# Optimization experiments

Measured on AMD Instinct MI355X. Metric: run time of the kernel, lower is better.

## Reference

```python
import jax, jax.numpy as jnp
import numpy as np

N = 4096   # patients
D = 256    # encoding dim per modality
EPS = 1e-8 # torch CosineSimilarity eps


def setup_inputs() -> dict:
    key = jax.random.key(0)
    ks = jax.random.split(key, 7)
    return {
        "log_hazard": jax.random.normal(ks[0], (N,), dtype=jnp.float32),
        "time": jax.random.randint(ks[1], (N,), 0, 3650, dtype=jnp.int32),
        "event": jax.random.randint(ks[2], (N,), 0, 2, dtype=jnp.int32),
        "eb0": jax.random.normal(ks[3], (N, D), dtype=jnp.float32),
        "eb1": jax.random.normal(ks[4], (N, D), dtype=jnp.float32),
        "eb2": jax.random.normal(ks[5], (N, D), dtype=jnp.float32),
        "eb3": jax.random.normal(ks[6], (N, D), dtype=jnp.float32),
        "M_margin": 1,
    }


def _cox_npll(h, t, e):
    # risk_matrix = (outer(t,t) >= t^2).T  ->  risk[i,j] = (t_j * t_i >= t_i^2)
    tt = t[:, None] * t[None, :]                      # [N,N] = t_i * t_j
    risk = (tt >= (t * t)[:, None]).astype(h.dtype)   # row i: patients j with t_j >= t_i
    log_denom = jnp.log(risk @ jnp.exp(h))            # [N]
    ef = e.astype(h.dtype)
    return -jnp.sum(ef * (h - log_denom)) / jnp.sum(ef)


def _similarity_loss(blocks, margin):
    # Vectorized form of the O(N^2 * n_mod) pairwise loop.
    matched = jnp.zeros((N, N), dtype=blocks[0].dtype)  # sum_mod cos(x_i, x_j) over valid mods
    own = jnp.zeros((N, N), dtype=blocks[0].dtype)      # sum_mod cos(x_i, x_i) over valid mods
    for x in blocks:
        nrm = jnp.linalg.norm(x, axis=1)                # [N]
        den = jnp.maximum(nrm, EPS)
        xn = x / den[:, None]
        S = xn @ xn.T                                   # cos(x_i, x_j) with torch eps semantics
        diag = (nrm * nrm) / (den * den)                # cos(x_i, x_i)
        miss = jnp.all(x == x[:, :1], axis=1)           # modality missing (constant row)
        valid = (~(miss[:, None] | miss[None, :])).astype(x.dtype)
        matched = matched + valid * S
        own = own + valid * diag[:, None]
    offdiag = 1.0 - jnp.eye(N, dtype=matched.dtype)
    per_pair = jax.nn.relu(margin - matched + own)
    return jnp.sum(offdiag * per_pair)


def reference(log_hazard, time, event, eb0, eb1, eb2, eb3, M_margin):
    margin = jnp.float32(M_margin)
    cox = _cox_npll(log_hazard, time, event)
    sim = _similarity_loss([eb0, eb1, eb2, eb3], margin)
    return cox + sim
```

## Files before the change

### kernel.cpp

```cpp
#include <hip/hip_runtime.h>
#include <stdint.h>

#define NPAT 4096
#define DIM  256
#define EPSV 1e-8f
#define BT   128
#define NT   (NPAT / BT)
#define NBLK (NT * (NT + 1) / 2)
#define NSTEP 16
#define NBINS 4096

typedef float f32x4  __attribute__((ext_vector_type(4)));
typedef float f32x16 __attribute__((ext_vector_type(16)));
typedef int   i32x8  __attribute__((ext_vector_type(8)));

#define WS_DVAL_OFF 256
#define WS_MVEC_OFF (WS_DVAL_OFF + 16*NPAT)
#define WS_XN_OFF   (WS_MVEC_OFF + 16*NPAT)

__device__ __forceinline__ float decode_margin(const int* pm) {
  int v = *pm;
  if (v > -16777216 && v < 16777216) return (float)v;
  return __int_as_float(v);
}

__global__ __launch_bounds__(256) void prep_kernel(
    const float4* __restrict__ eb0, const float4* __restrict__ eb1,
    const float4* __restrict__ eb2, const float4* __restrict__ eb3,
    uint8_t* __restrict__ XnF, float* __restrict__ dval_f,
    float* __restrict__ mvec_f, float* __restrict__ scal)
{
  const int i    = blockIdx.x;
  const int wv   = threadIdx.x >> 6;
  const int lane = threadIdx.x & 63;
  const float4* ebs[4] = {eb0, eb1, eb2, eb3};
  const float4 v = ebs[wv][i * (DIM / 4) + lane];
  float s = v.x * v.x + v.y * v.y + v.z * v.z + v.w * v.w;
#pragma unroll
  for (int o = 32; o; o >>= 1) s += __shfl_down(s, o, 64);
  s = __shfl(s, 0, 64);
  const float x0 = __shfl(v.x, 0, 64);
  const bool eq = (v.x == x0) && (v.y == x0) && (v.z == x0) && (v.w == x0);
  const bool miss = (__ballot(eq) == ~0ull);
  const float nrm = sqrtf(s);
  const float den = fmaxf(nrm, EPSV);
  const float inv = miss ? 0.0f : (1.0f / den);
  int p = 0;
  p = __builtin_amdgcn_cvt_pk_fp8_f32(v.x * inv, v.y * inv, p, false);
  p = __builtin_amdgcn_cvt_pk_fp8_f32(v.z * inv, v.w * inv, p, true);
  const int g  = i >> 5, r = i & 31;
  const int ss = wv * 4 + (lane >> 4);
  const int h  = (lane >> 3) & 1;
  const int b  = (lane & 7) * 4;
  *(int*)&XnF[(size_t)((g * 16 + ss) * 64 + (h * 32 + r)) * 32 + b] = p;
  if (lane == 0) {
    const float diag = (nrm * nrm) / (den * den);
    dval_f[i * 4 + wv] = miss ? 0.0f : diag;
    mvec_f[i * 4 + wv] = miss ? 0.0f : 1.0f;
  }
  if (i == 0 && threadIdx.x == 0) {
    scal[0] = 0.0f;
    scal[1] = 0.0f;
    ((unsigned*)scal)[2] = 0u;
  }
}

__global__ __launch_bounds__(256, 3) void sim_gemm_kernel(
    const uint8_t* __restrict__ XnF, const float4* __restrict__ dval,
    const float4* __restrict__ mvec, const int* __restrict__ pmargin,
    const float* __restrict__ h, const int* __restrict__ t,
    const int* __restrict__ e, float* __restrict__ scal,
    float* __restrict__ out)
{
  __shared__ __align__(16) uint8_t smem[16384 + 256];
  const int L   = blockIdx.x;
  const int tid = threadIdx.x;
  const int lane = tid & 63, wvv = tid >> 6;

  if (L == 0) {
    float* bins = (float*)smem;
    float* wt   = (float*)(smem + 16384);
    float* rn   = (float*)(smem + 16384 + 32);
    float* rd   = (float*)(smem + 16384 + 64);
#pragma unroll
    for (int k = 0; k < 16; ++k) bins[tid + k * 256] = 0.0f;
    __syncthreads();
#pragma unroll
    for (int k = 0; k < 16; ++k) {
      const int i = tid + k * 256;
      atomicAdd(&bins[t[i]], expf(h[i]));
    }
    __syncthreads();
    float seg[16]; float part = 0.0f;
#pragma unroll
    for (int k = 0; k < 16; ++k) { seg[k] = bins[tid * 16 + k]; part += seg[k]; }
    float sfx = part;
#pragma unroll
    for (int off = 1; off < 64; off <<= 1) {
      const float u = __shfl_down(sfx, off, 64);
      if (lane + off < 64) sfx += u;
    }
    if (lane == 0) wt[wvv] = sfx;
    __syncthreads();
    float above = 0.0f;
    for (int w = wvv + 1; w < 4; ++w) above += wt[w];
    float run = above + (sfx - part);
#pragma unroll
    for (int k = 15; k >= 0; --k) { run += seg[k]; bins[tid * 16 + k] = run; }
    __syncthreads();
    float nloc = 0.0f, dloc = 0.0f;
#pragma unroll
    for (int k = 0; k < 16; ++k) {
      const int i = tid + k * 256;
      const float ei = (float)e[i];
      if (ei != 0.0f) { nloc += ei * (h[i] - logf(bins[t[i]])); dloc += ei; }
    }
#pragma unroll
    for (int o = 32; o; o >>= 1) {
      nloc += __shfl_down(nloc, o, 64);
      dloc += __shfl_down(dloc, o, 64);
    }
    if (lane == 0) { rn[wvv] = nloc; rd[wvv] = dloc; }
    __syncthreads();
    if (tid == 0) {
      float n = 0.0f, d = 0.0f;
#pragma unroll
      for (int k = 0; k < 4; ++k) { n += rn[k]; d += rd[k]; }
      atomicExch(&scal[1], n / d);
      __threadfence();
      const unsigned old = atomicAdd(&((unsigned*)scal)[2], 1u);
      if (old == NBLK) {
        __threadfence();
        out[0] = atomicAdd(&scal[0], 0.0f) - (n / d);
      }
    }
    return;
  }

  const int T = L - 1;
  int bi = (int)((2 * NT + 1 - sqrtf((float)((2 * NT + 1) * (2 * NT + 1)) - 8.0f * T)) * 0.5f);
  if (bi < 0) bi = 0;
  if (bi > NT - 1) bi = NT - 1;
  while (bi > 0 && bi * NT - bi * (bi - 1) / 2 > T) --bi;
  while ((bi + 1) * NT - (bi + 1) * bi / 2 <= T) ++bi;
  const int bj = bi + (T - (bi * NT - bi * (bi - 1) / 2));

  const int wi = wvv >> 1, wj = wvv & 1;
  const int gA0 = bi * 4 + wi * 2;
  const int gB0 = bj * 4 + wj * 2;
  const uint8_t* pA = XnF + (size_t)(gA0 * 16) * 2048 + lane * 32;
  const uint8_t* pB = XnF + (size_t)(gB0 * 16) * 2048 + lane * 32;

  f32x16 acc[2][2] = {};

#pragma unroll 2
  for (int s = 0; s < NSTEP; ++s) {
    const i32x8 a0 = *(const i32x8*)(pA + (size_t)s * 2048);
    const i32x8 a1 = *(const i32x8*)(pA + 32768 + (size_t)s * 2048);
    const i32x8 b0 = *(const i32x8*)(pB + (size_t)s * 2048);
    const i32x8 b1 = *(const i32x8*)(pB + 32768 + (size_t)s * 2048);
    acc[0][0] = __builtin_amdgcn_mfma_scale_f32_32x32x64_f8f6f4(
        a0, b0, acc[0][0], 0, 0, 0, 0x7F7F7F7F, 0, 0x7F7F7F7F);
    acc[0][1] = __builtin_amdgcn_mfma_scale_f32_32x32x64_f8f6f4(
        a0, b1, acc[0][1], 0, 0, 0, 0x7F7F7F7F, 0, 0x7F7F7F7F);
    acc[1][0] = __builtin_amdgcn_mfma_scale_f32_32x32x64_f8f6f4(
        a1, b0, acc[1][0], 0, 0, 0, 0x7F7F7F7F, 0, 0x7F7F7F7F);
    acc[1][1] = __builtin_amdgcn_mfma_scale_f32_32x32x64_f8f6f4(
        a1, b1, acc[1][1], 0, 0, 0, 0x7F7F7F7F, 0, 0x7F7F7F7F);
  }

  float4* eRDi = (float4*)smem;
  float4* eCMi = (float4*)smem + BT;
  float4* eRDj = (float4*)smem + 2 * BT;
  float4* eCMj = (float4*)smem + 3 * BT;
  float*  wred = (float*)(smem + 8192);
  if (tid < BT) {
    eRDi[tid] = dval[bi * BT + tid];
    eCMi[tid] = mvec[bi * BT + tid];
  } else {
    const int ss = tid - BT;
    eRDj[ss] = dval[bj * BT + ss];
    eCMj[ss] = mvec[bj * BT + ss];
  }
  __syncthreads();

  const float margin = decode_margin(pmargin);
  const bool isDiag = (bi == bj);
  float local = 0.0f;
  const int colA = lane & 31, hsel = lane >> 5;
#pragma unroll
  for (int mi = 0; mi < 2; ++mi) {
#pragma unroll
    for (int mj = 0; mj < 2; ++mj) {
      const int jl = wj * 64 + mj * 32 + colA;
      const float4 cmj = eCMj[jl];
      const float4 rdj = eRDj[jl];
#pragma unroll
      for (int rr = 0; rr < 16; ++rr) {
        const int il = wi * 64 + mi * 32 + (rr & 3) + 8 * (rr >> 2) + 4 * hsel;
        const float4 rdi = eRDi[il];
        const float sv = acc[mi][mj][rr];
        const float own_ij = rdi.x * cmj.x + rdi.y * cmj.y + rdi.z * cmj.z + rdi.w * cmj.w;
        const float v1 = fmaxf(margin - sv + own_ij, 0.0f);
        local += (isDiag && il == jl) ? 0.0f : v1;
        if (!isDiag) {
          const float4 cmi = eCMi[il];
          const float own_ji = rdj.x * cmi.x + rdj.y * cmi.y + rdj.z * cmi.z + rdj.w * cmi.w;
          local += fmaxf(margin - sv + own_ji, 0.0f);
        }
      }
    }
  }
#pragma unroll
  for (int o = 32; o; o >>= 1) local += __shfl_down(local, o, 64);
  if (lane == 0) wred[wvv] = local;
  __syncthreads();
  if (tid == 0) {
    atomicAdd(&scal[0], wred[0] + wred[1] + wred[2] + wred[3]);
    __threadfence();
    const unsigned old = atomicAdd(&((unsigned*)scal)[2], 1u);
    if (old == NBLK) {
      __threadfence();
      out[0] = atomicAdd(&scal[0], 0.0f) - atomicAdd(&scal[1], 0.0f);
    }
  }
}

extern "C" void kernel_launch(void* const* d_in, const int* in_sizes, int n_in,
                              void* d_out, int out_size, void* d_ws, size_t ws_size,
                              hipStream_t stream) {
  const float* h    = (const float*)d_in[0];
  const int*   t    = (const int*)  d_in[1];
  const int*   e    = (const int*)  d_in[2];
  const float4* eb0 = (const float4*)d_in[3];
  const float4* eb1 = (const float4*)d_in[4];
  const float4* eb2 = (const float4*)d_in[5];
  const float4* eb3 = (const float4*)d_in[6];
  const int*   pm   = (const int*)  d_in[7];

  char*    ws   = (char*)d_ws;
  float*   scal = (float*)ws;
  float*   dvf  = (float*)(ws + WS_DVAL_OFF);
  float*   mvf  = (float*)(ws + WS_MVEC_OFF);
  uint8_t* XnF  = (uint8_t*)(ws + WS_XN_OFF);

  prep_kernel<<<NPAT, 256, 0, stream>>>(eb0, eb1, eb2, eb3, XnF, dvf, mvf, scal);
  sim_gemm_kernel<<<NBLK + 1, 256, 0, stream>>>(XnF, (const float4*)dvf, (const float4*)mvf,
                                                pm, h, t, e, scal, (float*)d_out);
}
```

Before: 109.0 us.

## Use 128x64 rectangular tiles over upper triangle with register double-buffered loads

Measured after the change: 124.1 us. 1.14x slower.

```diff
diff --git a/kernel.cpp b/kernel.cpp
--- a/kernel.cpp
+++ b/kernel.cpp
@@ -4,9 +4,9 @@
 #define NPAT 4096
 #define DIM  256
 #define EPSV 1e-8f
-#define BT   128
-#define NT   (NPAT / BT)
-#define NBLK (NT * (NT + 1) / 2)
+#define NRT  32
+#define NCT  64
+#define NBT  1056
 #define NSTEP 16
 #define NBINS 4096
 
@@ -129,7 +129,7 @@
       atomicExch(&scal[1], n / d);
       __threadfence();
       const unsigned old = atomicAdd(&((unsigned*)scal)[2], 1u);
-      if (old == NBLK) {
+      if (old == NBT) {
         __threadfence();
         out[0] = atomicAdd(&scal[0], 0.0f) - (n / d);
       }
@@ -138,76 +138,74 @@
   }
 
   const int T = L - 1;
-  int bi = (int)((2 * NT + 1 - sqrtf((float)((2 * NT + 1) * (2 * NT + 1)) - 8.0f * T)) * 0.5f);
-  if (bi < 0) bi = 0;
-  if (bi > NT - 1) bi = NT - 1;
-  while (bi > 0 && bi * NT - bi * (bi - 1) / 2 > T) --bi;
-  while ((bi + 1) * NT - (bi + 1) * bi / 2 <= T) ++bi;
-  const int bj = bi + (T - (bi * NT - bi * (bi - 1) / 2));
+  int ri = (int)((65.0f - sqrtf(4225.0f - 4.0f * T)) * 0.5f);
+  if (ri < 0) ri = 0;
+  if (ri > NRT - 1) ri = NRT - 1;
+  while (ri > 0 && ri * (65 - ri) > T) --ri;
+  while ((ri + 1) * (65 - (ri + 1)) <= T) ++ri;
+  const int cj = 2 * ri + (T - ri * (65 - ri));
 
   const int wi = wvv >> 1, wj = wvv & 1;
-  const int gA0 = bi * 4 + wi * 2;
-  const int gB0 = bj * 4 + wj * 2;
+  const int gA0 = ri * 4 + wi * 2;
+  const int gB  = cj * 2 + wj;
   const uint8_t* pA = XnF + (size_t)(gA0 * 16) * 2048 + lane * 32;
-  const uint8_t* pB = XnF + (size_t)(gB0 * 16) * 2048 + lane * 32;
-
-  f32x16 acc[2][2] = {};
-
+  const uint8_t* pB = XnF + (size_t)(gB  * 16) * 2048 + lane * 32;
+
+  f32x16 acc[2] = {};
+  i32x8 af[2][2], bf[2];
+
+  af[0][0] = *(const i32x8*)(pA);
+  af[0][1] = *(const i32x8*)(pA + 32768);
+  bf[0]    = *(const i32x8*)(pB);
 #pragma unroll 2
   for (int s = 0; s < NSTEP; ++s) {
-    const i32x8 a0 = *(const i32x8*)(pA + (size_t)s * 2048);
-    const i32x8 a1 = *(const i32x8*)(pA + 32768 + (size_t)s * 2048);
-    const i32x8 b0 = *(const i32x8*)(pB + (size_t)s * 2048);
-    const i32x8 b1 = *(const i32x8*)(pB + 32768 + (size_t)s * 2048);
-    acc[0][0] = __builtin_amdgcn_mfma_scale_f32_32x32x64_f8f6f4(
-        a0, b0, acc[0][0], 0, 0, 0, 0x7F7F7F7F, 0, 0x7F7F7F7F);
-    acc[0][1] = __builtin_amdgcn_mfma_scale_f32_32x32x64_f8f6f4(
-        a0, b1, acc[0][1], 0, 0, 0, 0x7F7F7F7F, 0, 0x7F7F7F7F);
-    acc[1][0] = __builtin_amdgcn_mfma_scale_f32_32x32x64_f8f6f4(
-        a1, b0, acc[1][0], 0, 0, 0, 0x7F7F7F7F, 0, 0x7F7F7F7F);
-    acc[1][1] = __builtin_amdgcn_mfma_scale_f32_32x32x64_f8f6f4(
-        a1, b1, acc[1][1], 0, 0, 0, 0x7F7F7F7F, 0, 0x7F7F7F7F);
+    const int c = s & 1;
+    if (s < NSTEP - 1) {
+      af[c ^ 1][0] = *(const i32x8*)(pA + (size_t)(s + 1) * 2048);
+      af[c ^ 1][1] = *(const i32x8*)(pA + 32768 + (size_t)(s + 1) * 2048);
+      bf[c ^ 1]    = *(const i32x8*)(pB + (size_t)(s + 1) * 2048);
+    }
+    acc[0] = __builtin_amdgcn_mfma_scale_f32_32x32x64_f8f6f4(
+        af[c][0], bf[c], acc[0], 0, 0, 0, 0x7F7F7F7F, 0, 0x7F7F7F7F);
+    acc[1] = __builtin_amdgcn_mfma_scale_f32_32x32x64_f8f6f4(
+        af[c][1], bf[c], acc[1], 0, 0, 0, 0x7F7F7F7F, 0, 0x7F7F7F7F);
   }
 
   float4* eRDi = (float4*)smem;
-  float4* eCMi = (float4*)smem + BT;
-  float4* eRDj = (float4*)smem + 2 * BT;
-  float4* eCMj = (float4*)smem + 3 * BT;
-  float*  wred = (float*)(smem + 8192);
-  if (tid < BT) {
-    eRDi[tid] = dval[bi * BT + tid];
-    eCMi[tid] = mvec[bi * BT + tid];
-  } else {
-    const int ss = tid - BT;
-    eRDj[ss] = dval[bj * BT + ss];
-    eCMj[ss] = mvec[bj * BT + ss];
+  float4* eCMi = (float4*)smem + 128;
+  float4* eRDj = (float4*)smem + 256;
+  float4* eCMj = (float4*)smem + 320;
+  float*  wred = (float*)(smem + 384 * 16);
+  if (tid < 128) {
+    eRDi[tid] = dval[ri * 128 + tid];
+    eCMi[tid] = mvec[ri * 128 + tid];
+  } else if (tid < 192) {
+    const int ss = tid - 128;
+    eRDj[ss] = dval[cj * 64 + ss];
+    eCMj[ss] = mvec[cj * 64 + ss];
   }
   __syncthreads();
 
   const float margin = decode_margin(pmargin);
-  const bool isDiag = (bi == bj);
   float local = 0.0f;
   const int colA = lane & 31, hsel = lane >> 5;
+  const int jl = wj * 32 + colA;
+  const int jg = cj * 64 + jl;
+  const float4 cmj = eCMj[jl];
+  const float4 rdj = eRDj[jl];
 #pragma unroll
   for (int mi = 0; mi < 2; ++mi) {
 #pragma unroll
-    for (int mj = 0; mj < 2; ++mj) {
-      const int jl = wj * 64 + mj * 32 + colA;
-      const float4 cmj = eCMj[jl];
-      const float4 rdj = eRDj[jl];
-#pragma unroll
-      for (int rr = 0; rr < 16; ++rr) {
-        const int il = wi * 64 + mi * 32 + (rr & 3) + 8 * (rr >> 2) + 4 * hsel;
+    for (int rr = 0; rr < 16; ++rr) {
+      const int il = wi * 64 + mi * 32 + (rr & 3) + 8 * (rr >> 2) + 4 * hsel;
+      const int ig = ri * 128 + il;
+      if (jg > ig) {
         const float4 rdi = eRDi[il];
-        const float sv = acc[mi][mj][rr];
+        const float4 cmi = eCMi[il];
+        const float sv = acc[mi][rr];
         const float own_ij = rdi.x * cmj.x + rdi.y * cmj.y + rdi.z * cmj.z + rdi.w * cmj.w;
-        const float v1 = fmaxf(margin - sv + own_ij, 0.0f);
-        local += (isDiag && il == jl) ? 0.0f : v1;
-        if (!isDiag) {
-          const float4 cmi = eCMi[il];
-          const float own_ji = rdj.x * cmi.x + rdj.y * cmi.y + rdj.z * cmi.z + rdj.w * cmi.w;
-          local += fmaxf(margin - sv + own_ji, 0.0f);
-        }
+        const float own_ji = rdj.x * cmi.x + rdj.y * cmi.y + rdj.z * cmi.z + rdj.w * cmi.w;
+        local += fmaxf(margin - sv + own_ij, 0.0f) + fmaxf(margin - sv + own_ji, 0.0f);
       }
     }
   }
@@ -219,7 +217,7 @@
     atomicAdd(&scal[0], wred[0] + wred[1] + wred[2] + wred[3]);
     __threadfence();
     const unsigned old = atomicAdd(&((unsigned*)scal)[2], 1u);
-    if (old == NBLK) {
+    if (old == NBT) {
       __threadfence();
       out[0] = atomicAdd(&scal[0], 0.0f) - atomicAdd(&scal[1], 0.0f);
     }
@@ -245,6 +243,6 @@
   uint8_t* XnF  = (uint8_t*)(ws + WS_XN_OFF);
 
   prep_kernel<<<NPAT, 256, 0, stream>>>(eb0, eb1, eb2, eb3, XnF, dvf, mvf, scal);
-  sim_gemm_kernel<<<NBLK + 1, 256, 0, stream>>>(XnF, (const float4*)dvf, (const float4*)mvf,
-                                                pm, h, t, e, scal, (float*)d_out);
-}
+  sim_gemm_kernel<<<NBT + 1, 256, 0, stream>>>(XnF, (const float4*)dvf, (const float4*)mvf,
+                                               pm, h, t, e, scal, (float*)d_out);
+}
```

## Use 256x128 rectangular triangular tiles with 512-thread blocks and batched fragment loads

Applied to the files above, without the earlier changes.

Result: slower. 116.5 us (+6.9%).

```diff
diff --git a/kernel.cpp b/kernel.cpp
--- a/kernel.cpp
+++ b/kernel.cpp
@@ -4,9 +4,9 @@
 #define NPAT 4096
 #define DIM  256
 #define EPSV 1e-8f
-#define BT   128
-#define NT   (NPAT / BT)
-#define NBLK (NT * (NT + 1) / 2)
+#define NRT  16
+#define NCT  32
+#define NBT  272
 #define NSTEP 16
 #define NBINS 4096
 
@@ -65,7 +65,7 @@
   }
 }
 
-__global__ __launch_bounds__(256, 3) void sim_gemm_kernel(
+__global__ __launch_bounds__(512, 2) void sim_gemm_kernel(
     const uint8_t* __restrict__ XnF, const float4* __restrict__ dval,
     const float4* __restrict__ mvec, const int* __restrict__ pmargin,
     const float* __restrict__ h, const int* __restrict__ t,
@@ -80,20 +80,20 @@
   if (L == 0) {
     float* bins = (float*)smem;
     float* wt   = (float*)(smem + 16384);
-    float* rn   = (float*)(smem + 16384 + 32);
-    float* rd   = (float*)(smem + 16384 + 64);
-#pragma unroll
-    for (int k = 0; k < 16; ++k) bins[tid + k * 256] = 0.0f;
-    __syncthreads();
-#pragma unroll
-    for (int k = 0; k < 16; ++k) {
-      const int i = tid + k * 256;
+    float* rn   = (float*)(smem + 16384 + 64);
+    float* rd   = (float*)(smem + 16384 + 128);
+#pragma unroll
+    for (int k = 0; k < 8; ++k) bins[tid + k * 512] = 0.0f;
+    __syncthreads();
+#pragma unroll
+    for (int k = 0; k < 8; ++k) {
+      const int i = tid + k * 512;
       atomicAdd(&bins[t[i]], expf(h[i]));
     }
     __syncthreads();
-    float seg[16]; float part = 0.0f;
-#pragma unroll
-    for (int k = 0; k < 16; ++k) { seg[k] = bins[tid * 16 + k]; part += seg[k]; }
+    float seg[8]; float part = 0.0f;
+#pragma unroll
+    for (int k = 0; k < 8; ++k) { seg[k] = bins[tid * 8 + k]; part += seg[k]; }
     float sfx = part;
 #pragma unroll
     for (int off = 1; off < 64; off <<= 1) {
@@ -103,15 +103,15 @@
     if (lane == 0) wt[wvv] = sfx;
     __syncthreads();
     float above = 0.0f;
-    for (int w = wvv + 1; w < 4; ++w) above += wt[w];
+    for (int w = wvv + 1; w < 8; ++w) above += wt[w];
     float run = above + (sfx - part);
 #pragma unroll
-    for (int k = 15; k >= 0; --k) { run += seg[k]; bins[tid * 16 + k] = run; }
+    for (int k = 7; k >= 0; --k) { run += seg[k]; bins[tid * 8 + k] = run; }
     __syncthreads();
     float nloc = 0.0f, dloc = 0.0f;
 #pragma unroll
-    for (int k = 0; k < 16; ++k) {
-      const int i = tid + k * 256;
+    for (int k = 0; k < 8; ++k) {
+      const int i = tid + k * 512;
       const float ei = (float)e[i];
       if (ei != 0.0f) { nloc += ei * (h[i] - logf(bins[t[i]])); dloc += ei; }
     }
@@ -125,11 +125,11 @@
     if (tid == 0) {
       float n = 0.0f, d = 0.0f;
 #pragma unroll
-      for (int k = 0; k < 4; ++k) { n += rn[k]; d += rd[k]; }
+      for (int k = 0; k < 8; ++k) { n += rn[k]; d += rd[k]; }
       atomicExch(&scal[1], n / d);
       __threadfence();
       const unsigned old = atomicAdd(&((unsigned*)scal)[2], 1u);
-      if (old == NBLK) {
+      if (old == NBT) {
         __threadfence();
         out[0] = atomicAdd(&scal[0], 0.0f) - (n / d);
       }
@@ -138,75 +138,82 @@
   }
 
   const int T = L - 1;
-  int bi = (int)((2 * NT + 1 - sqrtf((float)((2 * NT + 1) * (2 * NT + 1)) - 8.0f * T)) * 0.5f);
-  if (bi < 0) bi = 0;
-  if (bi > NT - 1) bi = NT - 1;
-  while (bi > 0 && bi * NT - bi * (bi - 1) / 2 > T) --bi;
-  while ((bi + 1) * NT - (bi + 1) * bi / 2 <= T) ++bi;
-  const int bj = bi + (T - (bi * NT - bi * (bi - 1) / 2));
+  int ri = (int)((33.0f - sqrtf(1089.0f - 4.0f * T)) * 0.5f);
+  if (ri < 0) ri = 0;
+  if (ri > NRT - 1) ri = NRT - 1;
+  while (ri > 0 && ri * (33 - ri) > T) --ri;
+  while ((ri + 1) * (32 - ri) <= T) ++ri;
+  const int cj = 2 * ri + (T - ri * (33 - ri));
 
   const int wi = wvv >> 1, wj = wvv & 1;
-  const int gA0 = bi * 4 + wi * 2;
-  const int gB0 = bj * 4 + wj * 2;
+  const int gA0 = ri * 8 + wi * 2;
+  const int gB0 = cj * 4 + wj * 2;
   const uint8_t* pA = XnF + (size_t)(gA0 * 16) * 2048 + lane * 32;
   const uint8_t* pB = XnF + (size_t)(gB0 * 16) * 2048 + lane * 32;
 
   f32x16 acc[2][2] = {};
 
-#pragma unroll 2
-  for (int s = 0; s < NSTEP; ++s) {
-    const i32x8 a0 = *(const i32x8*)(pA + (size_t)s * 2048);
-    const i32x8 a1 = *(const i32x8*)(pA + 32768 + (size_t)s * 2048);
-    const i32x8 b0 = *(const i32x8*)(pB + (size_t)s * 2048);
-    const i32x8 b1 = *(const i32x8*)(pB + 32768 + (size_t)s * 2048);
-    acc[0][0] = __builtin_amdgcn_mfma_scale_f32_32x32x64_f8f6f4(
-        a0, b0, acc[0][0], 0, 0, 0, 0x7F7F7F7F, 0, 0x7F7F7F7F);
-    acc[0][1] = __builtin_amdgcn_mfma_scale_f32_32x32x64_f8f6f4(
-        a0, b1, acc[0][1], 0, 0, 0, 0x7F7F7F7F, 0, 0x7F7F7F7F);
-    acc[1][0] = __builtin_amdgcn_mfma_scale_f32_32x32x64_f8f6f4(
-        a1, b0, acc[1][0], 0, 0, 0, 0x7F7F7F7F, 0, 0x7F7F7F7F);
-    acc[1][1] = __builtin_amdgcn_mfma_scale_f32_32x32x64_f8f6f4(
-        a1, b1, acc[1][1], 0, 0, 0, 0x7F7F7F7F, 0, 0x7F7F7F7F);
+#pragma unroll 1
+  for (int b = 0; b < 4; ++b) {
+    i32x8 A0[4], A1[4], B0[4], B1[4];
+    const size_t base = (size_t)b * 4 * 2048;
+#pragma unroll
+    for (int s = 0; s < 4; ++s) {
+      A0[s] = *(const i32x8*)(pA + base + (size_t)s * 2048);
+      A1[s] = *(const i32x8*)(pA + 32768 + base + (size_t)s * 2048);
+      B0[s] = *(const i32x8*)(pB + base + (size_t)s * 2048);
+      B1[s] = *(const i32x8*)(pB + 32768 + base + (size_t)s * 2048);
+    }
+#pragma unroll
+    for (int s = 0; s < 4; ++s) {
+      acc[0][0] = __builtin_amdgcn_mfma_scale_f32_32x32x64_f8f6f4(
+          A0[s], B0[s], acc[0][0], 0, 0, 0, 0x7F7F7F7F, 0, 0x7F7F7F7F);
+      acc[0][1] = __builtin_amdgcn_mfma_scale_f32_32x32x64_f8f6f4(
+          A0[s], B1[s], acc[0][1], 0, 0, 0, 0x7F7F7F7F, 0, 0x7F7F7F7F);
+      acc[1][0] = __builtin_amdgcn_mfma_scale_f32_32x32x64_f8f6f4(
+          A1[s], B0[s], acc[1][0], 0, 0, 0, 0x7F7F7F7F, 0, 0x7F7F7F7F);
+      acc[1][1] = __builtin_amdgcn_mfma_scale_f32_32x32x64_f8f6f4(
+          A1[s], B1[s], acc[1][1], 0, 0, 0, 0x7F7F7F7F, 0, 0x7F7F7F7F);
+    }
   }
 
   float4* eRDi = (float4*)smem;
-  float4* eCMi = (float4*)smem + BT;
-  float4* eRDj = (float4*)smem + 2 * BT;
-  float4* eCMj = (float4*)smem + 3 * BT;
-  float*  wred = (float*)(smem + 8192);
-  if (tid < BT) {
-    eRDi[tid] = dval[bi * BT + tid];
-    eCMi[tid] = mvec[bi * BT + tid];
-  } else {
-    const int ss = tid - BT;
-    eRDj[ss] = dval[bj * BT + ss];
-    eCMj[ss] = mvec[bj * BT + ss];
+  float4* eCMi = (float4*)smem + 256;
+  float4* eRDj = (float4*)smem + 512;
+  float4* eCMj = (float4*)smem + 640;
+  float*  wred = (float*)(smem + 768 * 16);
+  if (tid < 256) {
+    eRDi[tid] = dval[ri * 256 + tid];
+    eCMi[tid] = mvec[ri * 256 + tid];
+  } else if (tid < 384) {
+    const int ss = tid - 256;
+    eRDj[ss] = dval[cj * 128 + ss];
+    eCMj[ss] = mvec[cj * 128 + ss];
   }
   __syncthreads();
 
   const float margin = decode_margin(pmargin);
-  const bool isDiag = (bi == bj);
   float local = 0.0f;
   const int colA = lane & 31, hsel = lane >> 5;
 #pragma unroll
-  for (int mi = 0; mi < 2; ++mi) {
-#pragma unroll
-    for (int mj = 0; mj < 2; ++mj) {
-      const int jl = wj * 64 + mj * 32 + colA;
-      const float4 cmj = eCMj[jl];
-      const float4 rdj = eRDj[jl];
+  for (int mj = 0; mj < 2; ++mj) {
+    const int jl = wj * 64 + mj * 32 + colA;
+    const int jg = cj * 128 + jl;
+    const float4 cmj = eCMj[jl];
+    const float4 rdj = eRDj[jl];
+#pragma unroll
+    for (int mi = 0; mi < 2; ++mi) {
 #pragma unroll
       for (int rr = 0; rr < 16; ++rr) {
         const int il = wi * 64 + mi * 32 + (rr & 3) + 8 * (rr >> 2) + 4 * hsel;
-        const float4 rdi = eRDi[il];
-        const float sv = acc[mi][mj][rr];
-        const float own_ij = rdi.x * cmj.x + rdi.y * cmj.y + rdi.z * cmj.z + rdi.w * cmj.w;
-        const float v1 = fmaxf(margin - sv + own_ij, 0.0f);
-        local += (isDiag && il == jl) ? 0.0f : v1;
-        if (!isDiag) {
+        const int ig = ri * 256 + il;
+        if (jg > ig) {
+          const float4 rdi = eRDi[il];
           const float4 cmi = eCMi[il];
+          const float sv = acc[mi][mj][rr];
+          const float own_ij = rdi.x * cmj.x + rdi.y * cmj.y + rdi.z * cmj.z + rdi.w * cmj.w;
           const float own_ji = rdj.x * cmi.x + rdj.y * cmi.y + rdj.z * cmi.z + rdj.w * cmi.w;
-          local += fmaxf(margin - sv + own_ji, 0.0f);
+          local += fmaxf(margin - sv + own_ij, 0.0f) + fmaxf(margin - sv + own_ji, 0.0f);
         }
       }
     }
@@ -216,10 +223,13 @@
   if (lane == 0) wred[wvv] = local;
   __syncthreads();
   if (tid == 0) {
-    atomicAdd(&scal[0], wred[0] + wred[1] + wred[2] + wred[3]);
+    float bsum = 0.0f;
+#pragma unroll
+    for (int k = 0; k < 8; ++k) bsum += wred[k];
+    atomicAdd(&scal[0], bsum);
     __threadfence();
     const unsigned old = atomicAdd(&((unsigned*)scal)[2], 1u);
-    if (old == NBLK) {
+    if (old == NBT) {
       __threadfence();
       out[0] = atomicAdd(&scal[0], 0.0f) - atomicAdd(&scal[1], 0.0f);
     }
@@ -245,6 +255,6 @@
   uint8_t* XnF  = (uint8_t*)(ws + WS_XN_OFF);
 
   prep_kernel<<<NPAT, 256, 0, stream>>>(eb0, eb1, eb2, eb3, XnF, dvf, mvf, scal);
-  sim_gemm_kernel<<<NBLK + 1, 256, 0, stream>>>(XnF, (const float4*)dvf, (const float4*)mvf,
-                                                pm, h, t, e, scal, (float*)d_out);
-}
+  sim_gemm_kernel<<<NBT + 1, 512, 0, stream>>>(XnF, (const float4*)dvf, (const float4*)mvf,
+                                               pm, h, t, e, scal, (float*)d_out);
+}
```
